# Kernel tuning notes

Hardware: AMD Instinct MI355X
Metric: run time of the kernel (lower is better)

Reference implementation:

```python
import jax, jax.numpy as jnp
import numpy as np

MARGIN = 0.3


def setup_inputs() -> dict:
    key = jax.random.key(0)
    k1, k2 = jax.random.split(key)
    N, D = 8192, 128
    embeddings = jax.random.normal(k1, (N, D), dtype=jnp.float32)
    labels = jax.random.randint(k2, (N,), 0, 512, dtype=jnp.int64)
    return {"embeddings": embeddings, "labels": labels}


def _pairwise_dist(x):
    # Euclidean cdist via squared-norm expansion; safe sqrt (zero grad at d==0).
    sq_norms = jnp.sum(x * x, axis=-1)  # [N]
    sq = sq_norms[:, None] + sq_norms[None, :] - 2.0 * (x @ x.T)  # [N, N]
    sq = jnp.maximum(sq, 0.0)
    safe = jnp.where(sq > 0.0, sq, 1.0)
    return jnp.where(sq > 0.0, jnp.sqrt(safe), 0.0)


def reference(embeddings, labels):
    d = _pairwise_dist(embeddings)  # [N, N]
    same = labels[:, None] == labels[None, :]
    eye = jnp.eye(labels.shape[0], dtype=bool)
    pos_mask = same & ~eye
    neg_mask = ~same

    inf = jnp.float32(jnp.inf)
    hardest_pos = jnp.max(jnp.where(pos_mask, d, -inf), axis=1)  # [N]
    hardest_neg = jnp.min(jnp.where(neg_mask, d, inf), axis=1)   # [N]

    valid = jnp.any(pos_mask, axis=1) & jnp.any(neg_mask, axis=1)
    per_row = jax.nn.relu(hardest_pos - hardest_neg + MARGIN)
    per_row = jnp.where(valid, per_row, 0.0)
    count = jnp.sum(valid)
    return jnp.where(count > 0, jnp.sum(per_row) / jnp.maximum(count, 1), 0.0)
```

## Files before the change

kernel.cpp:

```cpp
#include <hip/hip_runtime.h>
#include <hip/hip_fp16.h>

#define N 8192
#define D 128
#define MARGIN 0.3f
#define NCHUNK 8
#define JTILES 8

typedef __fp16 half_t;
typedef __attribute__((ext_vector_type(8))) __fp16 half8;
typedef __attribute__((ext_vector_type(4))) float f32x4;

__global__ void triplet_prep(const float* __restrict__ x,
                             half_t* __restrict__ xh,
                             float* __restrict__ norms,
                             float* __restrict__ gacc) {
    const int gt = blockIdx.x * 256 + threadIdx.x;
    if (gt < 2) gacc[gt] = 0.f;
    const int row  = gt >> 6;
    const int lane = gt & 63;
    const float* rp = x + (size_t)row * D;
    float a0 = rp[lane], a1 = rp[lane + 64];
    xh[(size_t)row * D + lane]      = (half_t)a0;
    xh[(size_t)row * D + lane + 64] = (half_t)a1;
    float s = fmaf(a0, a0, a1 * a1);
#pragma unroll
    for (int o = 32; o > 0; o >>= 1) s += __shfl_xor(s, o);
    if (lane == 0) norms[row] = s;
}

__launch_bounds__(256, 2)
__global__ void triplet_main(const half_t* __restrict__ xh,
                             const float* __restrict__ norms,
                             const int* __restrict__ labels,
                             float* __restrict__ ppos,
                             float* __restrict__ pneg) {
    __shared__ __align__(16) half_t Ah[128 * 128];
    __shared__ __align__(16) half_t Bh[128 * 128];

    const int bx    = blockIdx.x;
    const int strip = bx >> 3;
    const int chunk = bx & 7;
    const int tid   = threadIdx.x;
    const int lane  = tid & 63;
    const int w     = tid >> 6;
    const int wr    = w >> 1;
    const int wc    = w & 1;
    const int lrow  = lane >> 4;
    const int lcol  = lane & 15;

    const int irow0 = strip * 128;

#pragma unroll
    for (int it = 0; it < 8; ++it) {
        int f = it * 256 + tid;
        int row = f >> 4, sp = f & 15;
        int sl = sp ^ (row & 7);
        *(uint4*)(Ah + f * 8) = *(const uint4*)(xh + (size_t)(irow0 + row) * D + sl * 8);
    }

    int physk[4];
#pragma unroll
    for (int ks = 0; ks < 4; ++ks) physk[ks] = ((ks * 4 + lrow) ^ (lcol & 7)) * 8;
    int rowA[4], rowB[4];
#pragma unroll
    for (int f4 = 0; f4 < 4; ++f4) {
        rowA[f4] = (wr * 64 + f4 * 16 + lcol) * D;
        rowB[f4] = (wc * 64 + f4 * 16 + lcol) * D;
    }

    const int ibase = irow0 + wr * 64 + lrow * 4;
    int li[16];
#pragma unroll
    for (int fi = 0; fi < 4; ++fi)
#pragma unroll
        for (int rg = 0; rg < 4; ++rg)
            li[fi * 4 + rg] = labels[ibase + fi * 16 + rg];

    float mpos[16], mneg[16];
#pragma unroll
    for (int r = 0; r < 16; ++r) { mpos[r] = -1e38f; mneg[r] = 1e38f; }

    for (int jt = 0; jt < JTILES; ++jt) {
        const int jbase = chunk * 1024 + jt * 128;
        __syncthreads();
#pragma unroll
        for (int it = 0; it < 8; ++it) {
            int f = it * 256 + tid;
            int row = f >> 4, sp = f & 15;
            int sl = sp ^ (row & 7);
            *(uint4*)(Bh + f * 8) = *(const uint4*)(xh + (size_t)(jbase + row) * D + sl * 8);
        }
        __syncthreads();

        int lj[4]; float njv[4];
#pragma unroll
        for (int fj = 0; fj < 4; ++fj) {
            int j = jbase + wc * 64 + fj * 16 + lcol;
            lj[fj]  = labels[j];
            njv[fj] = norms[j];
        }

        f32x4 acc[4][4];
#pragma unroll
        for (int fi = 0; fi < 4; ++fi)
#pragma unroll
            for (int fj = 0; fj < 4; ++fj)
                acc[fi][fj] = (f32x4){0.f, 0.f, 0.f, 0.f};

#pragma unroll
        for (int ks = 0; ks < 4; ++ks) {
            half8 av[4], bv[4];
#pragma unroll
            for (int fi = 0; fi < 4; ++fi)
                av[fi] = *(const half8*)(Ah + rowA[fi] + physk[ks]);
#pragma unroll
            for (int fj = 0; fj < 4; ++fj)
                bv[fj] = *(const half8*)(Bh + rowB[fj] + physk[ks]);
#pragma unroll
            for (int fi = 0; fi < 4; ++fi)
#pragma unroll
                for (int fj = 0; fj < 4; ++fj)
                    acc[fi][fj] = __builtin_amdgcn_mfma_f32_16x16x32_f16(
                        av[fi], bv[fj], acc[fi][fj], 0, 0, 0);
        }

        const bool hasdiag = (jbase == irow0);
        const int jcolbase = jbase + wc * 64 + lcol;
#pragma unroll
        for (int fi = 0; fi < 4; ++fi) {
#pragma unroll
            for (int fj = 0; fj < 4; ++fj) {
#pragma unroll
                for (int rg = 0; rg < 4; ++rg) {
                    float cand = fmaf(-2.f, acc[fi][fj][rg], njv[fj]);
                    int r = fi * 4 + rg;
                    bool same = (li[r] == lj[fj]);
                    bool pos = same;
                    if (hasdiag) {
                        int ig = ibase + fi * 16 + rg;
                        int jg = jcolbase + fj * 16;
                        pos = same && (ig != jg);
                    }
                    if (pos)   mpos[r] = fmaxf(mpos[r], cand);
                    if (!same) mneg[r] = fminf(mneg[r], cand);
                }
            }
        }
    }

#pragma unroll
    for (int o = 1; o < 16; o <<= 1) {
#pragma unroll
        for (int r = 0; r < 16; ++r) {
            mpos[r] = fmaxf(mpos[r], __shfl_xor(mpos[r], o));
            mneg[r] = fminf(mneg[r], __shfl_xor(mneg[r], o));
        }
    }
    if (lcol == 0) {
        const int slot = chunk * 2 + wc;
#pragma unroll
        for (int fi = 0; fi < 4; ++fi)
#pragma unroll
            for (int rg = 0; rg < 4; ++rg) {
                int rgrow = ibase + fi * 16 + rg;
                ppos[(size_t)rgrow * 16 + slot] = mpos[fi * 4 + rg];
                pneg[(size_t)rgrow * 16 + slot] = mneg[fi * 4 + rg];
            }
    }
}

__global__ void triplet_reduce(const float* __restrict__ ppos,
                               const float* __restrict__ pneg,
                               const float* __restrict__ norms,
                               float* __restrict__ gacc) {
    __shared__ float ss[256];
    __shared__ float sc[256];
    const int tid = threadIdx.x;
    const int r   = blockIdx.x * 256 + tid;
    float mp = -1e38f, mn = 1e38f;
    const f32x4* pp = (const f32x4*)(ppos + (size_t)r * 16);
    const f32x4* pn = (const f32x4*)(pneg + (size_t)r * 16);
#pragma unroll
    for (int s4 = 0; s4 < 4; ++s4) {
        f32x4 a = pp[s4], b = pn[s4];
#pragma unroll
        for (int e = 0; e < 4; ++e) { mp = fmaxf(mp, a[e]); mn = fminf(mn, b[e]); }
    }
    float ni = norms[r];
    bool valid = (mp > -1e37f) && (mn < 1e37f);
    float hp = sqrtf(fmaxf(ni + mp, 0.f));
    float hn = sqrtf(fmaxf(ni + mn, 0.f));
    float pr = fmaxf(hp - hn + MARGIN, 0.f);
    ss[tid] = valid ? pr : 0.f;
    sc[tid] = valid ? 1.f : 0.f;
    __syncthreads();
    for (int o = 128; o > 0; o >>= 1) {
        if (tid < o) { ss[tid] += ss[tid + o]; sc[tid] += sc[tid + o]; }
        __syncthreads();
    }
    if (tid == 0) { atomicAdd(&gacc[0], ss[0]); atomicAdd(&gacc[1], sc[0]); }
}

__global__ void triplet_final(const float* __restrict__ gacc, float* __restrict__ out) {
    out[0] = (gacc[1] > 0.f) ? (gacc[0] / gacc[1]) : 0.f;
}

extern "C" void kernel_launch(void* const* d_in, const int* in_sizes, int n_in,
                              void* d_out, int out_size, void* d_ws, size_t ws_size,
                              hipStream_t stream) {
    const float* x      = (const float*)d_in[0];
    const int*   labels = (const int*)d_in[1];
    float*       out    = (float*)d_out;

    char*   ws    = (char*)d_ws;
    half_t* xh    = (half_t*)ws;
    float*  norms = (float*)(ws + (size_t)N * D * sizeof(half_t));
    float*  ppos  = norms + N;
    float*  pneg  = ppos + (size_t)N * 16;
    float*  gacc  = pneg + (size_t)N * 16;

    triplet_prep  <<<N / 4,   256, 0, stream>>>(x, xh, norms, gacc);
    triplet_main  <<<512,     256, 0, stream>>>(xh, norms, labels, ppos, pneg);
    triplet_reduce<<<N / 256, 256, 0, stream>>>(ppos, pneg, norms, gacc);
    triplet_final <<<1,       1,   0, stream>>>(gacc, out);
}
```

Measured before the change: 46.59 us.

## Double-buffer B tiles via direct global-to-LDS loads and hold A in registers

The main kernel now uses global_load_lds to copy the next 128-row B tile straight into LDS while the current tile is multiplied, with two LDS buffers swapped each iteration. The A tile is loaded once into registers after its first LDS staging, so it is not re-read from LDS on every k-step. The final one-thread kernel is folded into the reduce kernel through an atomic ticket counter, removing one launch. The cost is higher register pressure from holding A fragments, and the pipeline depends on hand-placed waitcnt and barrier instructions being correct.

```diff
diff --git a/kernel.cpp b/kernel.cpp
--- a/kernel.cpp
+++ b/kernel.cpp
@@ -4,19 +4,20 @@
 #define N 8192
 #define D 128
 #define MARGIN 0.3f
-#define NCHUNK 8
-#define JTILES 8
 
 typedef __fp16 half_t;
 typedef __attribute__((ext_vector_type(8))) __fp16 half8;
 typedef __attribute__((ext_vector_type(4))) float f32x4;
+
+#define AS1C(p) ((const __attribute__((address_space(1))) void*)(p))
+#define AS3(p)  ((__attribute__((address_space(3))) void*)(p))
 
 __global__ void triplet_prep(const float* __restrict__ x,
                              half_t* __restrict__ xh,
                              float* __restrict__ norms,
                              float* __restrict__ gacc) {
     const int gt = blockIdx.x * 256 + threadIdx.x;
-    if (gt < 2) gacc[gt] = 0.f;
+    if (gt < 3) gacc[gt] = 0.f;
     const int row  = gt >> 6;
     const int lane = gt & 63;
     const float* rp = x + (size_t)row * D;
@@ -35,8 +36,7 @@
                              const int* __restrict__ labels,
                              float* __restrict__ ppos,
                              float* __restrict__ pneg) {
-    __shared__ __align__(16) half_t Ah[128 * 128];
-    __shared__ __align__(16) half_t Bh[128 * 128];
+    __shared__ __align__(16) half_t S[2][128 * D];
 
     const int bx    = blockIdx.x;
     const int strip = bx >> 3;
@@ -48,26 +48,11 @@
     const int wc    = w & 1;
     const int lrow  = lane >> 4;
     const int lcol  = lane & 15;
-
     const int irow0 = strip * 128;
 
-#pragma unroll
-    for (int it = 0; it < 8; ++it) {
-        int f = it * 256 + tid;
-        int row = f >> 4, sp = f & 15;
-        int sl = sp ^ (row & 7);
-        *(uint4*)(Ah + f * 8) = *(const uint4*)(xh + (size_t)(irow0 + row) * D + sl * 8);
-    }
-
-    int physk[4];
-#pragma unroll
-    for (int ks = 0; ks < 4; ++ks) physk[ks] = ((ks * 4 + lrow) ^ (lcol & 7)) * 8;
-    int rowA[4], rowB[4];
-#pragma unroll
-    for (int f4 = 0; f4 < 4; ++f4) {
-        rowA[f4] = (wr * 64 + f4 * 16 + lcol) * D;
-        rowB[f4] = (wc * 64 + f4 * 16 + lcol) * D;
-    }
+    const int ssl   = (tid & 15) ^ ((tid >> 4) & 7);
+    const int sgoff = (tid >> 4) * D + ssl * 8;
+    const int sldst = tid * 8;
 
     const int ibase = irow0 + wr * 64 + lrow * 4;
     int li[16];
@@ -77,21 +62,56 @@
         for (int rg = 0; rg < 4; ++rg)
             li[fi * 4 + rg] = labels[ibase + fi * 16 + rg];
 
+#pragma unroll
+    for (int it = 0; it < 8; ++it)
+        __builtin_amdgcn_global_load_lds(AS1C(xh + (size_t)(irow0 + it * 16) * D + sgoff),
+                                         AS3(&S[0][it * 2048 + sldst]), 16, 0, 0);
+    const int jchunk0 = chunk * 1024;
+#pragma unroll
+    for (int it = 0; it < 8; ++it)
+        __builtin_amdgcn_global_load_lds(AS1C(xh + (size_t)(jchunk0 + it * 16) * D + sgoff),
+                                         AS3(&S[1][it * 2048 + sldst]), 16, 0, 0);
+    asm volatile("s_waitcnt vmcnt(0)" ::: "memory");
+    __builtin_amdgcn_s_barrier();
+    __builtin_amdgcn_sched_barrier(0);
+
+    int physk[4];
+#pragma unroll
+    for (int ks = 0; ks < 4; ++ks) physk[ks] = ((ks * 4 + lrow) ^ (lcol & 7)) * 8;
+    half8 af[4][4];
+#pragma unroll
+    for (int fi = 0; fi < 4; ++fi) {
+        const half_t* ap = &S[0][(wr * 64 + fi * 16 + lcol) * D];
+#pragma unroll
+        for (int ks = 0; ks < 4; ++ks)
+            af[fi][ks] = *(const half8*)(ap + physk[ks]);
+    }
+    asm volatile("s_waitcnt lgkmcnt(0)" ::: "memory");
+    __builtin_amdgcn_sched_barrier(0);
+    __builtin_amdgcn_s_barrier();
+    __builtin_amdgcn_sched_barrier(0);
+
+    int rowB[4];
+#pragma unroll
+    for (int f4 = 0; f4 < 4; ++f4) rowB[f4] = (wc * 64 + f4 * 16 + lcol) * D;
+
     float mpos[16], mneg[16];
 #pragma unroll
     for (int r = 0; r < 16; ++r) { mpos[r] = -1e38f; mneg[r] = 1e38f; }
 
-    for (int jt = 0; jt < JTILES; ++jt) {
-        const int jbase = chunk * 1024 + jt * 128;
-        __syncthreads();
-#pragma unroll
-        for (int it = 0; it < 8; ++it) {
-            int f = it * 256 + tid;
-            int row = f >> 4, sp = f & 15;
-            int sl = sp ^ (row & 7);
-            *(uint4*)(Bh + f * 8) = *(const uint4*)(xh + (size_t)(jbase + row) * D + sl * 8);
-        }
-        __syncthreads();
+    const half_t* Bcur  = &S[1][0];
+    half_t*       Bnext = &S[0][0];
+
+    for (int jt = 0; jt < 8; ++jt) {
+        const int jbase = jchunk0 + jt * 128;
+
+        if (jt < 7) {
+            const int nb = jbase + 128;
+#pragma unroll
+            for (int it = 0; it < 8; ++it)
+                __builtin_amdgcn_global_load_lds(AS1C(xh + (size_t)(nb + it * 16) * D + sgoff),
+                                                 AS3(Bnext + it * 2048 + sldst), 16, 0, 0);
+        }
 
         int lj[4]; float njv[4];
 #pragma unroll
@@ -110,19 +130,16 @@
 
 #pragma unroll
         for (int ks = 0; ks < 4; ++ks) {
-            half8 av[4], bv[4];
-#pragma unroll
-            for (int fi = 0; fi < 4; ++fi)
-                av[fi] = *(const half8*)(Ah + rowA[fi] + physk[ks]);
+            half8 bv[4];
 #pragma unroll
             for (int fj = 0; fj < 4; ++fj)
-                bv[fj] = *(const half8*)(Bh + rowB[fj] + physk[ks]);
+                bv[fj] = *(const half8*)(Bcur + rowB[fj] + physk[ks]);
 #pragma unroll
             for (int fi = 0; fi < 4; ++fi)
 #pragma unroll
                 for (int fj = 0; fj < 4; ++fj)
                     acc[fi][fj] = __builtin_amdgcn_mfma_f32_16x16x32_f16(
-                        av[fi], bv[fj], acc[fi][fj], 0, 0, 0);
+                        af[fi][ks], bv[fj], acc[fi][fj], 0, 0, 0);
         }
 
         const bool hasdiag = (jbase == irow0);
@@ -147,6 +164,11 @@
                 }
             }
         }
+
+        asm volatile("s_waitcnt vmcnt(0)" ::: "memory");
+        __builtin_amdgcn_s_barrier();
+        __builtin_amdgcn_sched_barrier(0);
+        const half_t* t = Bcur; Bcur = Bnext; Bnext = (half_t*)t;
     }
 
 #pragma unroll
@@ -173,7 +195,8 @@
 __global__ void triplet_reduce(const float* __restrict__ ppos,
                                const float* __restrict__ pneg,
                                const float* __restrict__ norms,
-                               float* __restrict__ gacc) {
+                               float* __restrict__ gacc,
+                               float* __restrict__ out) {
     __shared__ float ss[256];
     __shared__ float sc[256];
     const int tid = threadIdx.x;
@@ -199,11 +222,18 @@
         if (tid < o) { ss[tid] += ss[tid + o]; sc[tid] += sc[tid + o]; }
         __syncthreads();
     }
-    if (tid == 0) { atomicAdd(&gacc[0], ss[0]); atomicAdd(&gacc[1], sc[0]); }
-}
-
-__global__ void triplet_final(const float* __restrict__ gacc, float* __restrict__ out) {
-    out[0] = (gacc[1] > 0.f) ? (gacc[0] / gacc[1]) : 0.f;
+    if (tid == 0) {
+        atomicAdd(&gacc[0], ss[0]);
+        atomicAdd(&gacc[1], sc[0]);
+        __threadfence();
+        unsigned* ticket = (unsigned*)(gacc + 2);
+        unsigned old = atomicAdd(ticket, 1u);
+        if (old == gridDim.x - 1) {
+            float s = atomicAdd(&gacc[0], 0.f);
+            float c = atomicAdd(&gacc[1], 0.f);
+            out[0] = (c > 0.f) ? (s / c) : 0.f;
+        }
+    }
 }
 
 extern "C" void kernel_launch(void* const* d_in, const int* in_sizes, int n_in,
@@ -222,6 +252,5 @@
 
     triplet_prep  <<<N / 4,   256, 0, stream>>>(x, xh, norms, gacc);
     triplet_main  <<<512,     256, 0, stream>>>(xh, norms, labels, ppos, pneg);
-    triplet_reduce<<<N / 256, 256, 0, stream>>>(ppos, pneg, norms, gacc);
-    triplet_final <<<1,       1,   0, stream>>>(gacc, out);
-}
+    triplet_reduce<<<N / 256, 256, 0, stream>>>(ppos, pneg, norms, gacc, out);
+}
```

New measurement: 48.16 us. +3.4%, slower.
